# Optimization experiments

Hardware: AMD Instinct MI355X
Metric: run time of the kernel (lower is better)

The kernel has to match this reference:

```python
import jax, jax.numpy as jnp
import numpy as np

B, L, D = 4, 2048, 512
H, DK = 8, 64          # n_heads, d_k = d_model // n_heads
DF = 2048              # d_ff
W = 9                  # window_size (odd so padding w//2 keeps L windows)


def setup_inputs() -> dict:
    key = jax.random.key(0)
    ks = jax.random.split(key, 12)
    s = 0.02
    p = lambda k, shp: (jax.random.normal(k, shp, jnp.float32) * s)
    return {
        "x": jax.random.normal(ks[0], (B, L, D), jnp.float32),
        "Wq": p(ks[1], (D, D)), "bq": jnp.zeros((D,), jnp.float32),
        "Wk": p(ks[2], (D, D)), "bk": jnp.zeros((D,), jnp.float32),
        "Wv": p(ks[3], (D, D)), "bv": jnp.zeros((D,), jnp.float32),
        "Wo": p(ks[4], (D, D)), "bo": jnp.zeros((D,), jnp.float32),
        "W1": p(ks[5], (D, DF)), "b1": jnp.zeros((DF,), jnp.float32),
        "W2": p(ks[6], (DF, D)), "b2": jnp.zeros((D,), jnp.float32),
        "g1": jnp.ones((D,), jnp.float32), "be1": jnp.zeros((D,), jnp.float32),
        "g2": jnp.ones((D,), jnp.float32), "be2": jnp.zeros((D,), jnp.float32),
    }


def _layer_norm(x, g, b, eps=1e-5):
    m = jnp.mean(x, axis=-1, keepdims=True)
    v = jnp.var(x, axis=-1, keepdims=True)
    return (x - m) * jax.lax.rsqrt(v + eps) * g + b


def reference(x, Wq, bq, Wk, bk, Wv, bv, Wo, bo, W1, b1, W2, b2, g1, be1, g2, be2):
    b, l, d = x.shape
    pad = W // 2
    padded = jnp.pad(x, ((0, 0), (pad, pad), (0, 0)))          # (B, L+W-1, D)
    idx = jnp.arange(l)[:, None] + jnp.arange(W)[None, :]       # (L, W)
    win = padded[:, idx]                                        # (B, L, W, D)

    # per-window full attention (Informer FullAttention, mask_flag=False)
    q = (win @ Wq + bq).reshape(b, l, W, H, DK)
    k = (win @ Wk + bk).reshape(b, l, W, H, DK)
    v = (win @ Wv + bv).reshape(b, l, W, H, DK)
    scale = 1.0 / jnp.sqrt(jnp.float32(DK))
    scores = jnp.einsum('blqhe,blkhe->blhqk', q, k) * scale     # (B, L, H, W, W)
    attn = jax.nn.softmax(scores, axis=-1)
    o = jnp.einsum('blhqk,blkhd->blqhd', attn, v).reshape(b, l, W, d)
    o = o @ Wo + bo                                             # (B, L, W, D)
    new_x = jnp.mean(o, axis=2)                                 # mean-pool over window

    x1 = _layer_norm(x + new_x, g1, be1)

    # pointwise conv FFN (kernel_size=1 Conv1d == Linear), exact GELU
    h = jax.nn.gelu(x1 @ W1 + b1, approximate=False)
    y = h @ W2 + b2
    return _layer_norm(x1 + y, g2, be2)
```

## Files before the change

### kernel.cpp

```cpp
#include <hip/hip_runtime.h>


typedef unsigned short u16;
typedef __attribute__((ext_vector_type(8))) short short8;
typedef __attribute__((ext_vector_type(4))) float floatx4;

#define DEV static __device__ __forceinline__

DEV float b2f(u16 u) {
  union { unsigned int i; float f; } x; x.i = ((unsigned int)u) << 16; return x.f;
}
DEV u16 f2b(float f) {
  union { float f; unsigned int i; } x; x.f = f;
  unsigned int u = x.i + 0x7fffu + ((x.i >> 16) & 1u);
  return (u16)(u >> 16);
}

#define AS1 __attribute__((address_space(1)))
#define AS3 __attribute__((address_space(3)))
DEV void gload_lds16(const void* g, void* l) {
  __builtin_amdgcn_global_load_lds((const AS1 void*)g, (AS3 void*)l, 16, 0, 0);
}

__global__ __launch_bounds__(256) void prep_all(
    const float* __restrict__ Wq, const float* __restrict__ Wk,
    const float* __restrict__ Wo, const float* __restrict__ W1,
    const float* __restrict__ W2, const float* __restrict__ Wv,
    const float* __restrict__ bq, const float* __restrict__ bk,
    const float* __restrict__ bv, const float* __restrict__ x,
    u16* __restrict__ WqkvT, u16* __restrict__ WoT,
    u16* __restrict__ W1T, u16* __restrict__ W2T, u16* __restrict__ Wvb,
    float* __restrict__ bqkv, u16* __restrict__ xb) {
  const int bid = blockIdx.x;
  if (bid >= 3080) {
    const int i = (bid - 3080) * 256 + threadIdx.x;
    float4 v = ((const float4*)x)[i];
    ushort4 o;
    o.x = f2b(v.x); o.y = f2b(v.y); o.z = f2b(v.z); o.w = f2b(v.w);
    ((ushort4*)xb)[i] = o;
    return;
  }
  if (bid >= 3072) {
    const int i = (bid - 3072) * 256 + threadIdx.x;
    if (i < 512) bqkv[i] = bq[i];
    else if (i < 1024) bqkv[i] = bk[i - 512];
    else if (i < 1536) {
      const int c = i - 1024;
      float s = 0.f;
      for (int j = 0; j < 512; ++j) s += bv[j] * Wo[(size_t)j * 512 + c];
      bqkv[i] = s;
    } else bqkv[i] = 0.f;
    return;
  }
  if (bid >= 2816) {
    const int i = (bid - 2816) * 256 + threadIdx.x;
    float4 v = ((const float4*)Wv)[i];
    ushort4 o;
    o.x = f2b(v.x); o.y = f2b(v.y); o.z = f2b(v.z); o.w = f2b(v.w);
    ((ushort4*)Wvb)[i] = o;
    return;
  }
  const float* in; u16* out; int R, C, t;
  if (bid < 256)       { in = Wq; out = WqkvT;          R = 512;  C = 512;  t = bid; }
  else if (bid < 512)  { in = Wk; out = WqkvT + 262144; R = 512;  C = 512;  t = bid - 256; }
  else if (bid < 768)  { in = Wo; out = WoT;            R = 512;  C = 512;  t = bid - 512; }
  else if (bid < 1792) { in = W1; out = W1T;            R = 512;  C = 2048; t = bid - 768; }
  else                 { in = W2; out = W2T;            R = 2048; C = 512;  t = bid - 1792; }
  const int tpr = C >> 5;
  const int bc = (t % tpr) * 32, br = (t / tpr) * 32;
  __shared__ float tile[32][33];
  const int tx = threadIdx.x & 31, ty = threadIdx.x >> 5;
  #pragma unroll
  for (int i = 0; i < 32; i += 8)
    tile[ty + i][tx] = in[(size_t)(br + ty + i) * C + bc + tx];
  __syncthreads();
  #pragma unroll
  for (int i = 0; i < 32; i += 8)
    out[(size_t)(bc + ty + i) * R + br + tx] = f2b(tile[tx][ty + i]);
}

template<int EPI>
__global__ __launch_bounds__(256, 3) void gemm_bt(
    const u16* __restrict__ A, const u16* __restrict__ BT,
    const float* __restrict__ bias, u16* __restrict__ C,
    int M, int N, int lda, int kb) {
  __shared__ __align__(16) u16 As[2][8192];
  __shared__ __align__(16) u16 Bs[2][4096];
  const int tid = threadIdx.x;
  const int w = tid >> 6, l = tid & 63;
  const int l15 = l & 15, l4 = l >> 4;
  const int wr = w & 1, wc = w >> 1;

  const int gx = (int)gridDim.x, gy = (int)gridDim.y;
  int id = (int)blockIdx.y * gx + (int)blockIdx.x;
  const int nwg = gx * gy;
  if ((nwg & 7) == 0) { const int cpx = nwg >> 3; id = (id & 7) * cpx + (id >> 3); }
  const int bx = id % gx; const int by = id / gx;
  const int bm = by * 128, bn = bx * 64;

  const int srow = tid >> 3;
  const int sg8 = (((tid & 7) - (srow & 7)) & 7) * 8;
  const u16* gA = A  + (size_t)(bm + srow) * lda + sg8;
  const u16* gB = BT + (size_t)(bn + srow) * lda + sg8;
  const size_t r32 = (size_t)32 * lda;
  const int sd = tid * 8;

  int aOff[2][4], bOff[2][2];
  #pragma unroll
  for (int kh = 0; kh < 2; ++kh) {
    #pragma unroll
    for (int m = 0; m < 4; ++m) {
      const int r = wr * 64 + m * 16 + l15;
      aOff[kh][m] = r * 64 + (((l4 + 4 * kh) + (r & 7)) & 7) * 8;
    }
    #pragma unroll
    for (int n = 0; n < 2; ++n) {
      const int r = wc * 32 + n * 16 + l15;
      bOff[kh][n] = r * 64 + (((l4 + 4 * kh) + (r & 7)) & 7) * 8;
    }
  }

  floatx4 acc[4][2] = {};
  const int nt = kb >> 6;

  auto stage = [&](int t, int buf) {
    const u16* a = gA + (size_t)t * 64;
    const u16* b = gB + (size_t)t * 64;
    gload_lds16(a,           &As[buf][sd]);
    gload_lds16(a + r32,     &As[buf][2048 + sd]);
    gload_lds16(a + 2 * r32, &As[buf][4096 + sd]);
    gload_lds16(a + 3 * r32, &As[buf][6144 + sd]);
    gload_lds16(b,           &Bs[buf][sd]);
    gload_lds16(b + r32,     &Bs[buf][2048 + sd]);
  };

  stage(0, 0);
  asm volatile("s_waitcnt vmcnt(0)" ::: "memory");
  __builtin_amdgcn_s_barrier();
  asm volatile("" ::: "memory");

  for (int t = 0; t < nt; ++t) {
    const int cur = t & 1;
    if (t + 1 < nt) stage(t + 1, cur ^ 1);

    #pragma unroll
    for (int kh = 0; kh < 2; ++kh) {
      short8 af[4], bf[2];
      #pragma unroll
      for (int m = 0; m < 4; ++m) af[m] = *(const short8*)(&As[cur][aOff[kh][m]]);
      #pragma unroll
      for (int n = 0; n < 2; ++n) bf[n] = *(const short8*)(&Bs[cur][bOff[kh][n]]);
      #pragma unroll
      for (int m = 0; m < 4; ++m)
        #pragma unroll
        for (int n = 0; n < 2; ++n)
          acc[m][n] = __builtin_amdgcn_mfma_f32_16x16x32_bf16(af[m], bf[n], acc[m][n], 0, 0, 0);
    }

    asm volatile("s_waitcnt vmcnt(0)" ::: "memory");
    __builtin_amdgcn_s_barrier();
    asm volatile("" ::: "memory");
  }

  const int col0 = bn + wc * 32 + l15;
  float bvv[2];
  #pragma unroll
  for (int n = 0; n < 2; ++n) bvv[n] = bias[col0 + n * 16];
  #pragma unroll
  for (int m = 0; m < 4; ++m) {
    #pragma unroll
    for (int ri = 0; ri < 4; ++ri) {
      const size_t row = (size_t)(bm + wr * 64 + m * 16 + l4 * 4 + ri);
      u16* cp = C + row * N + col0;
      #pragma unroll
      for (int n = 0; n < 2; ++n) {
        float vv = acc[m][n][ri] + bvv[n];
        if (EPI == 1) {
          const float u = vv * (1.0f + 0.044715f * vv * vv);
          vv = vv / (1.0f + __expf(-1.5957691216057308f * u));
        }
        cp[n * 16] = f2b(vv);
      }
    }
  }
}

#define ATL 32
#define ART (ATL + 8)

__global__ __launch_bounds__(256) void attn_band(
    const u16* __restrict__ QKV, const float* __restrict__ bqkv,
    const float* __restrict__ bo, u16* __restrict__ newx) {
  __shared__ __align__(16) u16 S3[3][ART][72];
  __shared__ float Gb[ART][18];
  __shared__ float Sm[ART][81];
  __shared__ float Wb[ATL][9];

  const int tid = threadIdx.x;
  const int bid = ((int)blockIdx.x & 7) * 256 + ((int)blockIdx.x >> 3);
  const int h = bid & 7;
  const int chunk = (bid >> 3) & 63;
  const int b = bid >> 9;
  const int l0 = chunk * ATL;

  for (int idx = tid; idx < ART * 24; idx += 256) {
    const int ti = idx / 24, c = idx % 24;
    const int slice = c >> 3, d8 = (c & 7) * 8;
    const int col = slice * 512 + h * 64 + d8;
    const int t = l0 - 4 + ti;
    short8 v;
    if ((unsigned)t < 2048u) {
      v = *(const short8*)(QKV + ((size_t)((b << 11) | t)) * 1536 + col);
    } else {
      #pragma unroll
      for (int j = 0; j < 8; ++j) v[j] = (short)f2b(bqkv[col + j]);
    }
    *(short8*)(&S3[slice][ti][d8]) = v;
  }
  __syncthreads();

  for (int task = tid; task < ART * 17; task += 256) {
    const int ti = task / 17, j = task % 17;
    const int ui = ti + j - 8;
    if ((unsigned)ui < (unsigned)ART) {
      float a = 0.f;
      #pragma unroll
      for (int d0 = 0; d0 < 64; d0 += 8) {
        short8 qv = *(const short8*)(&S3[0][ti][d0]);
        short8 kv = *(const short8*)(&S3[1][ui][d0]);
        #pragma unroll
        for (int jj = 0; jj < 8; ++jj) a += b2f((u16)qv[jj]) * b2f((u16)kv[jj]);
      }
      Gb[ti][j] = a * 0.125f;
    }
  }
  __syncthreads();

  for (int task = tid; task < ART * 9; task += 256) {
    const int ti = task / 9, qw = task % 9;
    const int li = ti - qw;
    if ((unsigned)li < (unsigned)ATL) {
      float m = -1e30f;
      #pragma unroll
      for (int kw = 0; kw < 9; ++kw) m = fmaxf(m, Gb[ti][kw - qw + 8]);
      float e[9], s = 0.f;
      #pragma unroll
      for (int kw = 0; kw < 9; ++kw) { e[kw] = expf(Gb[ti][kw - qw + 8] - m); s += e[kw]; }
      const float inv = 1.f / s;
      #pragma unroll
      for (int kw = 0; kw < 9; ++kw) Sm[ti][qw * 9 + kw] = e[kw] * inv;
    }
  }
  __syncthreads();

  for (int task = tid; task < ATL * 9; task += 256) {
    const int li = task / 9, kw = task % 9;
    float s = 0.f;
    #pragma unroll
    for (int qw = 0; qw < 9; ++qw) s += Sm[li + qw][qw * 9 + kw];
    Wb[li][kw] = s * (1.f / 9.f);
  }
  __syncthreads();

  {
    const int li = tid >> 3, d8 = (tid & 7) * 8;
    float w[9];
    #pragma unroll
    for (int kw = 0; kw < 9; ++kw) w[kw] = Wb[li][kw];
    float a[8] = {};
    #pragma unroll
    for (int kw = 0; kw < 9; ++kw) {
      short8 vv = *(const short8*)(&S3[2][li + kw][d8]);
      #pragma unroll
      for (int jj = 0; jj < 8; ++jj) a[jj] += w[kw] * b2f((u16)vv[jj]);
    }
    short8 o;
    #pragma unroll
    for (int jj = 0; jj < 8; ++jj) o[jj] = (short)f2b(a[jj] + bo[h * 64 + d8 + jj]);
    const int l = l0 + li;
    *(short8*)(newx + ((size_t)((b << 11) | l)) * 512 + h * 64 + d8) = o;
  }
}

template<int MODE>
__global__ __launch_bounds__(256) void ln_kernel(
    const u16* __restrict__ a, const u16* __restrict__ bsrc,
    const float* __restrict__ g, const float* __restrict__ be,
    u16* __restrict__ outb, float* __restrict__ outf) {
  const int wave = threadIdx.x >> 6, lane = threadIdx.x & 63;
  const size_t row = (size_t)blockIdx.x * 4 + wave;
  const size_t base = row * 512 + lane * 8;
  const int gi = lane * 8;
  float v[8];
  short8 a8 = *(const short8*)(a + base);
  short8 b8 = *(const short8*)(bsrc + base);
  #pragma unroll
  for (int j = 0; j < 8; ++j) v[j] = b2f((u16)a8[j]) + b2f((u16)b8[j]);

  float s = 0.f;
  #pragma unroll
  for (int j = 0; j < 8; ++j) s += v[j];
  #pragma unroll
  for (int off = 32; off >= 1; off >>= 1) s += __shfl_xor(s, off, 64);
  const float mean = s * (1.f / 512.f);
  float sq = 0.f;
  #pragma unroll
  for (int j = 0; j < 8; ++j) { float d = v[j] - mean; sq += d * d; }
  #pragma unroll
  for (int off = 32; off >= 1; off >>= 1) sq += __shfl_xor(sq, off, 64);
  const float rs = rsqrtf(sq * (1.f / 512.f) + 1e-5f);

  if (MODE == 0) {
    short8 o;
    #pragma unroll
    for (int j = 0; j < 8; ++j)
      o[j] = (short)f2b((v[j] - mean) * rs * g[gi + j] + be[gi + j]);
    *(short8*)(outb + base) = o;
  } else {
    float4 o0, o1;
    o0.x = (v[0] - mean) * rs * g[gi + 0] + be[gi + 0];
    o0.y = (v[1] - mean) * rs * g[gi + 1] + be[gi + 1];
    o0.z = (v[2] - mean) * rs * g[gi + 2] + be[gi + 2];
    o0.w = (v[3] - mean) * rs * g[gi + 3] + be[gi + 3];
    o1.x = (v[4] - mean) * rs * g[gi + 4] + be[gi + 4];
    o1.y = (v[5] - mean) * rs * g[gi + 5] + be[gi + 5];
    o1.z = (v[6] - mean) * rs * g[gi + 6] + be[gi + 6];
    o1.w = (v[7] - mean) * rs * g[gi + 7] + be[gi + 7];
    *(float4*)(outf + base) = o0;
    *(float4*)(outf + base + 4) = o1;
  }
}

extern "C" void kernel_launch(void* const* d_in, const int* in_sizes, int n_in,
                              void* d_out, int out_size, void* d_ws, size_t ws_size,
                              hipStream_t stream) {
  const float* x   = (const float*)d_in[0];
  const float* Wq  = (const float*)d_in[1];
  const float* bq  = (const float*)d_in[2];
  const float* Wk  = (const float*)d_in[3];
  const float* bk  = (const float*)d_in[4];
  const float* Wv  = (const float*)d_in[5];
  const float* bv  = (const float*)d_in[6];
  const float* Wo  = (const float*)d_in[7];
  const float* bo  = (const float*)d_in[8];
  const float* W1  = (const float*)d_in[9];
  const float* b1  = (const float*)d_in[10];
  const float* W2  = (const float*)d_in[11];
  const float* b2  = (const float*)d_in[12];
  const float* g1  = (const float*)d_in[13];
  const float* be1 = (const float*)d_in[14];
  const float* g2  = (const float*)d_in[15];
  const float* be2 = (const float*)d_in[16];

  char* w = (char*)d_ws;
  u16*   xb    = (u16*)  (w + 0);
  u16*   WqkvT = (u16*)  (w + 8388608);
  u16*   WoT   = (u16*)  (w + 9961472);
  u16*   W1T   = (u16*)  (w + 10485760);
  u16*   W2T   = (u16*)  (w + 12582912);
  float* bqkv  = (float*)(w + 14680064);
  u16*   Wvb   = (u16*)  (w + 14688256);
  u16*   QKV   = (u16*)  (w + 15212544);
  u16*   hbuf  = QKV;
  u16*   newx  = (u16*)  (w + 48766976);
  u16*   x1b   = (u16*)  (w + 57155584);
  u16*   WvoT  = WqkvT + 524288;
  u16*   ybuf  = newx;

  prep_all<<<7176, 256, 0, stream>>>(Wq, Wk, Wo, W1, W2, Wv, bq, bk, bv, x,
                                     WqkvT, WoT, W1T, W2T, Wvb, bqkv, xb);
  gemm_bt<0><<<dim3(8, 4), 256, 0, stream>>>(WoT, Wvb, bqkv + 1536, WvoT,
                                             512, 512, 512, 512);
  gemm_bt<0><<<dim3(24, 64), 256, 0, stream>>>(xb, WqkvT, bqkv, QKV,
                                               8192, 1536, 512, 512);
  attn_band<<<2048, 256, 0, stream>>>(QKV, bqkv, bo, newx);
  ln_kernel<0><<<2048, 256, 0, stream>>>(xb, newx, g1, be1, x1b, nullptr);
  gemm_bt<1><<<dim3(32, 64), 256, 0, stream>>>(x1b, W1T, b1, hbuf,
                                               8192, 2048, 512, 512);
  gemm_bt<0><<<dim3(8, 64), 256, 0, stream>>>(hbuf, W2T, b2, ybuf,
                                              8192, 512, 2048, 2048);
  ln_kernel<1><<<2048, 256, 0, stream>>>(x1b, ybuf, g2, be2, nullptr, (float*)d_out);
}
```

Measured before the change: 145.0 us.

## Enlarge GEMM tiles to 256x128 and split-K the FFN down-projection

Replaces the 128x64 GEMM tile (BK=64) with a 256x128 tile (BK=32), where each wave holds an 8x4 MFMA accumulator block, so more MFMA work is done per LDS load. The second FFN GEMM (K=2048) is split into two K halves across gridDim.z, which writes two bf16 partial outputs. The final layernorm kernel sums those partials and adds the bias. This is meant to raise arithmetic intensity and keep enough blocks for the small-N GEMM, at the cost of more registers, lower occupancy, fewer blocks on the other GEMMs, and extra partial-sum traffic with bf16 rounding of each partial.

```diff
diff --git a/kernel.cpp b/kernel.cpp
--- a/kernel.cpp
+++ b/kernel.cpp
@@ -80,9 +80,9 @@
 }
 
 template<int EPI>
-__global__ __launch_bounds__(256, 3) void gemm_bt(
+__global__ __launch_bounds__(256, 2) void gemm_big(
     const u16* __restrict__ A, const u16* __restrict__ BT,
-    const float* __restrict__ bias, u16* __restrict__ C,
+    const float* __restrict__ bias, u16* __restrict__ C, u16* __restrict__ C2,
     int M, int N, int lda, int kb) {
   __shared__ __align__(16) u16 As[2][8192];
   __shared__ __align__(16) u16 Bs[2][4096];
@@ -92,46 +92,40 @@
   const int wr = w & 1, wc = w >> 1;
 
   const int gx = (int)gridDim.x, gy = (int)gridDim.y;
-  int id = (int)blockIdx.y * gx + (int)blockIdx.x;
-  const int nwg = gx * gy;
+  int id = ((int)blockIdx.z * gy + (int)blockIdx.y) * gx + (int)blockIdx.x;
+  const int nwg = gx * gy * (int)gridDim.z;
   if ((nwg & 7) == 0) { const int cpx = nwg >> 3; id = (id & 7) * cpx + (id >> 3); }
-  const int bx = id % gx; const int by = id / gx;
-  const int bm = by * 128, bn = bx * 64;
-
-  const int srow = tid >> 3;
-  const int sg8 = (((tid & 7) - (srow & 7)) & 7) * 8;
-  const u16* gA = A  + (size_t)(bm + srow) * lda + sg8;
-  const u16* gB = BT + (size_t)(bn + srow) * lda + sg8;
-  const size_t r32 = (size_t)32 * lda;
+  const int bx = id % gx; const int r1 = id / gx;
+  const int by = r1 % gy; const int bz = r1 / gy;
+  const int bm = by * 256, bn = bx * 128;
+  const int koff = bz * kb;
+
+  const int row0 = tid >> 2;
+  const int kc0 = ((((tid & 3) - ((tid >> 3) & 3)) & 3)) * 8;
+  const u16* gA = A  + (size_t)(bm + row0) * lda + koff + kc0;
+  const u16* gB = BT + (size_t)(bn + row0) * lda + koff + kc0;
+  const size_t r64 = (size_t)64 * lda;
   const int sd = tid * 8;
 
-  int aOff[2][4], bOff[2][2];
-  #pragma unroll
-  for (int kh = 0; kh < 2; ++kh) {
-    #pragma unroll
-    for (int m = 0; m < 4; ++m) {
-      const int r = wr * 64 + m * 16 + l15;
-      aOff[kh][m] = r * 64 + (((l4 + 4 * kh) + (r & 7)) & 7) * 8;
-    }
-    #pragma unroll
-    for (int n = 0; n < 2; ++n) {
-      const int r = wc * 32 + n * 16 + l15;
-      bOff[kh][n] = r * 64 + (((l4 + 4 * kh) + (r & 7)) & 7) * 8;
-    }
-  }
-
-  floatx4 acc[4][2] = {};
-  const int nt = kb >> 6;
+  const int rg8 = ((l4 + ((l15 >> 1) & 3)) & 3) * 8;
+  int aOff[8], bOff[4];
+  #pragma unroll
+  for (int m = 0; m < 8; ++m) aOff[m] = (wr * 128 + m * 16 + l15) * 32 + rg8;
+  #pragma unroll
+  for (int n = 0; n < 4; ++n) bOff[n] = (wc * 64 + n * 16 + l15) * 32 + rg8;
+
+  floatx4 acc[8][4] = {};
+  const int nt = kb >> 5;
 
   auto stage = [&](int t, int buf) {
-    const u16* a = gA + (size_t)t * 64;
-    const u16* b = gB + (size_t)t * 64;
+    const u16* a = gA + (size_t)t * 32;
+    const u16* b = gB + (size_t)t * 32;
     gload_lds16(a,           &As[buf][sd]);
-    gload_lds16(a + r32,     &As[buf][2048 + sd]);
-    gload_lds16(a + 2 * r32, &As[buf][4096 + sd]);
-    gload_lds16(a + 3 * r32, &As[buf][6144 + sd]);
+    gload_lds16(a + r64,     &As[buf][2048 + sd]);
+    gload_lds16(a + 2 * r64, &As[buf][4096 + sd]);
+    gload_lds16(a + 3 * r64, &As[buf][6144 + sd]);
     gload_lds16(b,           &Bs[buf][sd]);
-    gload_lds16(b + r32,     &Bs[buf][2048 + sd]);
+    gload_lds16(b + r64,     &Bs[buf][2048 + sd]);
   };
 
   stage(0, 0);
@@ -143,43 +137,54 @@
     const int cur = t & 1;
     if (t + 1 < nt) stage(t + 1, cur ^ 1);
 
-    #pragma unroll
-    for (int kh = 0; kh < 2; ++kh) {
-      short8 af[4], bf[2];
-      #pragma unroll
-      for (int m = 0; m < 4; ++m) af[m] = *(const short8*)(&As[cur][aOff[kh][m]]);
-      #pragma unroll
-      for (int n = 0; n < 2; ++n) bf[n] = *(const short8*)(&Bs[cur][bOff[kh][n]]);
-      #pragma unroll
-      for (int m = 0; m < 4; ++m)
-        #pragma unroll
-        for (int n = 0; n < 2; ++n)
-          acc[m][n] = __builtin_amdgcn_mfma_f32_16x16x32_bf16(af[m], bf[n], acc[m][n], 0, 0, 0);
-    }
+    short8 af[8], bf[4];
+    #pragma unroll
+    for (int m = 0; m < 8; ++m) af[m] = *(const short8*)(&As[cur][aOff[m]]);
+    #pragma unroll
+    for (int n = 0; n < 4; ++n) bf[n] = *(const short8*)(&Bs[cur][bOff[n]]);
+    #pragma unroll
+    for (int m = 0; m < 8; ++m)
+      #pragma unroll
+      for (int n = 0; n < 4; ++n)
+        acc[m][n] = __builtin_amdgcn_mfma_f32_16x16x32_bf16(af[m], bf[n], acc[m][n], 0, 0, 0);
 
     asm volatile("s_waitcnt vmcnt(0)" ::: "memory");
     __builtin_amdgcn_s_barrier();
     asm volatile("" ::: "memory");
   }
 
-  const int col0 = bn + wc * 32 + l15;
-  float bvv[2];
-  #pragma unroll
-  for (int n = 0; n < 2; ++n) bvv[n] = bias[col0 + n * 16];
-  #pragma unroll
-  for (int m = 0; m < 4; ++m) {
-    #pragma unroll
-    for (int ri = 0; ri < 4; ++ri) {
-      const size_t row = (size_t)(bm + wr * 64 + m * 16 + l4 * 4 + ri);
-      u16* cp = C + row * N + col0;
-      #pragma unroll
-      for (int n = 0; n < 2; ++n) {
-        float vv = acc[m][n][ri] + bvv[n];
-        if (EPI == 1) {
-          const float u = vv * (1.0f + 0.044715f * vv * vv);
-          vv = vv / (1.0f + __expf(-1.5957691216057308f * u));
+  const int col0 = bn + wc * 64 + l15;
+  if (EPI <= 1) {
+    float bvv[4];
+    #pragma unroll
+    for (int n = 0; n < 4; ++n) bvv[n] = bias[col0 + n * 16];
+    #pragma unroll
+    for (int m = 0; m < 8; ++m) {
+      #pragma unroll
+      for (int ri = 0; ri < 4; ++ri) {
+        const size_t row = (size_t)(bm + wr * 128 + m * 16 + l4 * 4 + ri);
+        u16* cp = C + row * N + col0;
+        #pragma unroll
+        for (int n = 0; n < 4; ++n) {
+          float vv = acc[m][n][ri] + bvv[n];
+          if (EPI == 1) {
+            const float u = vv * (1.0f + 0.044715f * vv * vv);
+            vv = vv / (1.0f + __expf(-1.5957691216057308f * u));
+          }
+          cp[n * 16] = f2b(vv);
         }
-        cp[n * 16] = f2b(vv);
+      }
+    }
+  } else {
+    u16* o = (bz == 0) ? C : C2;
+    #pragma unroll
+    for (int m = 0; m < 8; ++m) {
+      #pragma unroll
+      for (int ri = 0; ri < 4; ++ri) {
+        const size_t row = (size_t)(bm + wr * 128 + m * 16 + l4 * 4 + ri);
+        u16* cp = o + row * N + col0;
+        #pragma unroll
+        for (int n = 0; n < 4; ++n) cp[n * 16] = f2b(acc[m][n][ri]);
       }
     }
   }
@@ -285,6 +290,7 @@
 template<int MODE>
 __global__ __launch_bounds__(256) void ln_kernel(
     const u16* __restrict__ a, const u16* __restrict__ bsrc,
+    const u16* __restrict__ csrc, const float* __restrict__ bias,
     const float* __restrict__ g, const float* __restrict__ be,
     u16* __restrict__ outb, float* __restrict__ outf) {
   const int wave = threadIdx.x >> 6, lane = threadIdx.x & 63;
@@ -296,6 +302,11 @@
   short8 b8 = *(const short8*)(bsrc + base);
   #pragma unroll
   for (int j = 0; j < 8; ++j) v[j] = b2f((u16)a8[j]) + b2f((u16)b8[j]);
+  if (MODE == 1) {
+    short8 c8 = *(const short8*)(csrc + base);
+    #pragma unroll
+    for (int j = 0; j < 8; ++j) v[j] += b2f((u16)c8[j]) + bias[gi + j];
+  }
 
   float s = 0.f;
   #pragma unroll
@@ -365,19 +376,20 @@
   u16*   newx  = (u16*)  (w + 48766976);
   u16*   x1b   = (u16*)  (w + 57155584);
   u16*   WvoT  = WqkvT + 524288;
-  u16*   ybuf  = newx;
+  u16*   yp0   = newx;
+  u16*   yp1   = xb;
 
   prep_all<<<7176, 256, 0, stream>>>(Wq, Wk, Wo, W1, W2, Wv, bq, bk, bv, x,
                                      WqkvT, WoT, W1T, W2T, Wvb, bqkv, xb);
-  gemm_bt<0><<<dim3(8, 4), 256, 0, stream>>>(WoT, Wvb, bqkv + 1536, WvoT,
-                                             512, 512, 512, 512);
-  gemm_bt<0><<<dim3(24, 64), 256, 0, stream>>>(xb, WqkvT, bqkv, QKV,
-                                               8192, 1536, 512, 512);
+  gemm_big<0><<<dim3(4, 2, 1), 256, 0, stream>>>(WoT, Wvb, bqkv + 1536, WvoT, nullptr,
+                                                 512, 512, 512, 512);
+  gemm_big<0><<<dim3(12, 32, 1), 256, 0, stream>>>(xb, WqkvT, bqkv, QKV, nullptr,
+                                                   8192, 1536, 512, 512);
   attn_band<<<2048, 256, 0, stream>>>(QKV, bqkv, bo, newx);
-  ln_kernel<0><<<2048, 256, 0, stream>>>(xb, newx, g1, be1, x1b, nullptr);
-  gemm_bt<1><<<dim3(32, 64), 256, 0, stream>>>(x1b, W1T, b1, hbuf,
-                                               8192, 2048, 512, 512);
-  gemm_bt<0><<<dim3(8, 64), 256, 0, stream>>>(hbuf, W2T, b2, ybuf,
-                                              8192, 512, 2048, 2048);
-  ln_kernel<1><<<2048, 256, 0, stream>>>(x1b, ybuf, g2, be2, nullptr, (float*)d_out);
-}
+  ln_kernel<0><<<2048, 256, 0, stream>>>(xb, newx, nullptr, nullptr, g1, be1, x1b, nullptr);
+  gemm_big<1><<<dim3(16, 32, 1), 256, 0, stream>>>(x1b, W1T, b1, hbuf, nullptr,
+                                                   8192, 2048, 512, 512);
+  gemm_big<2><<<dim3(4, 32, 2), 256, 0, stream>>>(hbuf, W2T, nullptr, yp0, yp1,
+                                                  8192, 512, 2048, 1024);
+  ln_kernel<1><<<2048, 256, 0, stream>>>(x1b, yp0, yp1, b2, g2, be2, nullptr, (float*)d_out);
+}
```

After: 164.9 us. 13.7% more time.

## Split-K the W2 GEMM and load B fragments directly into registers

Applied to the files above, without the earlier changes.

The GEMM kernel no longer stages B tiles in LDS. Each wave loads its B fragments straight from global memory into registers, prefetched one K-step ahead. A grid z-dimension adds split-K: the W2 GEMM now runs as two K halves that write bf16 partials to two buffers, and the second LayerNorm sums both partials and adds the bias. This doubles the block count of the narrow W2 GEMM to improve occupancy and halves LDS use per block. The cost is extra partial-buffer traffic, an extra bf16 rounding of partial sums, and uncoalesced global B loads.

```diff
diff --git a/kernel.cpp b/kernel.cpp
--- a/kernel.cpp
+++ b/kernel.cpp
@@ -82,104 +82,135 @@
 template<int EPI>
 __global__ __launch_bounds__(256, 3) void gemm_bt(
     const u16* __restrict__ A, const u16* __restrict__ BT,
-    const float* __restrict__ bias, u16* __restrict__ C,
+    const float* __restrict__ bias, u16* __restrict__ C, u16* __restrict__ C2,
     int M, int N, int lda, int kb) {
   __shared__ __align__(16) u16 As[2][8192];
-  __shared__ __align__(16) u16 Bs[2][4096];
   const int tid = threadIdx.x;
   const int w = tid >> 6, l = tid & 63;
   const int l15 = l & 15, l4 = l >> 4;
   const int wr = w & 1, wc = w >> 1;
 
   const int gx = (int)gridDim.x, gy = (int)gridDim.y;
-  int id = (int)blockIdx.y * gx + (int)blockIdx.x;
-  const int nwg = gx * gy;
+  int id = ((int)blockIdx.z * gy + (int)blockIdx.y) * gx + (int)blockIdx.x;
+  const int nwg = gx * gy * (int)gridDim.z;
   if ((nwg & 7) == 0) { const int cpx = nwg >> 3; id = (id & 7) * cpx + (id >> 3); }
-  const int bx = id % gx; const int by = id / gx;
+  const int bx = id % gx; const int r1 = id / gx;
+  const int by = r1 % gy; const int bz = r1 / gy;
   const int bm = by * 128, bn = bx * 64;
+  const int koff = bz * kb;
 
   const int srow = tid >> 3;
   const int sg8 = (((tid & 7) - (srow & 7)) & 7) * 8;
-  const u16* gA = A  + (size_t)(bm + srow) * lda + sg8;
-  const u16* gB = BT + (size_t)(bn + srow) * lda + sg8;
+  const u16* gA = A + (size_t)(bm + srow) * lda + koff + sg8;
   const size_t r32 = (size_t)32 * lda;
   const int sd = tid * 8;
 
-  int aOff[2][4], bOff[2][2];
-  #pragma unroll
-  for (int kh = 0; kh < 2; ++kh) {
+  int aOff[2][4];
+  #pragma unroll
+  for (int kh = 0; kh < 2; ++kh)
     #pragma unroll
     for (int m = 0; m < 4; ++m) {
       const int r = wr * 64 + m * 16 + l15;
       aOff[kh][m] = r * 64 + (((l4 + 4 * kh) + (r & 7)) & 7) * 8;
     }
-    #pragma unroll
-    for (int n = 0; n < 2; ++n) {
-      const int r = wc * 32 + n * 16 + l15;
-      bOff[kh][n] = r * 64 + (((l4 + 4 * kh) + (r & 7)) & 7) * 8;
-    }
-  }
+
+  const u16* pB = BT + (size_t)(bn + wc * 32 + l15) * lda + koff + l4 * 8;
+  const size_t bn16 = (size_t)16 * lda;
 
   floatx4 acc[4][2] = {};
   const int nt = kb >> 6;
 
-  auto stage = [&](int t, int buf) {
+  auto stageA = [&](int t, int buf) {
     const u16* a = gA + (size_t)t * 64;
-    const u16* b = gB + (size_t)t * 64;
     gload_lds16(a,           &As[buf][sd]);
     gload_lds16(a + r32,     &As[buf][2048 + sd]);
     gload_lds16(a + 2 * r32, &As[buf][4096 + sd]);
     gload_lds16(a + 3 * r32, &As[buf][6144 + sd]);
-    gload_lds16(b,           &Bs[buf][sd]);
-    gload_lds16(b + r32,     &Bs[buf][2048 + sd]);
   };
 
-  stage(0, 0);
+  short8 b00, b01, b10, b11, n00, n01, n10, n11;
+  b00 = *(const short8*)(pB);
+  b01 = *(const short8*)(pB + bn16);
+  b10 = *(const short8*)(pB + 32);
+  b11 = *(const short8*)(pB + bn16 + 32);
+
+  stageA(0, 0);
   asm volatile("s_waitcnt vmcnt(0)" ::: "memory");
   __builtin_amdgcn_s_barrier();
   asm volatile("" ::: "memory");
 
   for (int t = 0; t < nt; ++t) {
     const int cur = t & 1;
-    if (t + 1 < nt) stage(t + 1, cur ^ 1);
-
-    #pragma unroll
-    for (int kh = 0; kh < 2; ++kh) {
-      short8 af[4], bf[2];
-      #pragma unroll
-      for (int m = 0; m < 4; ++m) af[m] = *(const short8*)(&As[cur][aOff[kh][m]]);
-      #pragma unroll
-      for (int n = 0; n < 2; ++n) bf[n] = *(const short8*)(&Bs[cur][bOff[kh][n]]);
-      #pragma unroll
-      for (int m = 0; m < 4; ++m)
-        #pragma unroll
-        for (int n = 0; n < 2; ++n)
-          acc[m][n] = __builtin_amdgcn_mfma_f32_16x16x32_bf16(af[m], bf[n], acc[m][n], 0, 0, 0);
+    const bool pf = (t + 1 < nt);
+    if (pf) {
+      stageA(t + 1, cur ^ 1);
+      const u16* pb = pB + (size_t)(t + 1) * 64;
+      n00 = *(const short8*)(pb);
+      n01 = *(const short8*)(pb + bn16);
+      n10 = *(const short8*)(pb + 32);
+      n11 = *(const short8*)(pb + bn16 + 32);
+    }
+
+    {
+      short8 af[4];
+      #pragma unroll
+      for (int m = 0; m < 4; ++m) af[m] = *(const short8*)(&As[cur][aOff[0][m]]);
+      #pragma unroll
+      for (int m = 0; m < 4; ++m) {
+        acc[m][0] = __builtin_amdgcn_mfma_f32_16x16x32_bf16(af[m], b00, acc[m][0], 0, 0, 0);
+        acc[m][1] = __builtin_amdgcn_mfma_f32_16x16x32_bf16(af[m], b01, acc[m][1], 0, 0, 0);
+      }
+    }
+    {
+      short8 af[4];
+      #pragma unroll
+      for (int m = 0; m < 4; ++m) af[m] = *(const short8*)(&As[cur][aOff[1][m]]);
+      #pragma unroll
+      for (int m = 0; m < 4; ++m) {
+        acc[m][0] = __builtin_amdgcn_mfma_f32_16x16x32_bf16(af[m], b10, acc[m][0], 0, 0, 0);
+        acc[m][1] = __builtin_amdgcn_mfma_f32_16x16x32_bf16(af[m], b11, acc[m][1], 0, 0, 0);
+      }
     }
 
     asm volatile("s_waitcnt vmcnt(0)" ::: "memory");
     __builtin_amdgcn_s_barrier();
     asm volatile("" ::: "memory");
+
+    if (pf) { b00 = n00; b01 = n01; b10 = n10; b11 = n11; }
   }
 
   const int col0 = bn + wc * 32 + l15;
-  float bvv[2];
-  #pragma unroll
-  for (int n = 0; n < 2; ++n) bvv[n] = bias[col0 + n * 16];
-  #pragma unroll
-  for (int m = 0; m < 4; ++m) {
-    #pragma unroll
-    for (int ri = 0; ri < 4; ++ri) {
-      const size_t row = (size_t)(bm + wr * 64 + m * 16 + l4 * 4 + ri);
-      u16* cp = C + row * N + col0;
-      #pragma unroll
-      for (int n = 0; n < 2; ++n) {
-        float vv = acc[m][n][ri] + bvv[n];
-        if (EPI == 1) {
-          const float u = vv * (1.0f + 0.044715f * vv * vv);
-          vv = vv / (1.0f + __expf(-1.5957691216057308f * u));
+  if (EPI <= 1) {
+    float bvv[2];
+    #pragma unroll
+    for (int n = 0; n < 2; ++n) bvv[n] = bias[col0 + n * 16];
+    #pragma unroll
+    for (int m = 0; m < 4; ++m) {
+      #pragma unroll
+      for (int ri = 0; ri < 4; ++ri) {
+        const size_t row = (size_t)(bm + wr * 64 + m * 16 + l4 * 4 + ri);
+        u16* cp = C + row * N + col0;
+        #pragma unroll
+        for (int n = 0; n < 2; ++n) {
+          float vv = acc[m][n][ri] + bvv[n];
+          if (EPI == 1) {
+            const float u = vv * (1.0f + 0.044715f * vv * vv);
+            vv = vv / (1.0f + __expf(-1.5957691216057308f * u));
+          }
+          cp[n * 16] = f2b(vv);
         }
-        cp[n * 16] = f2b(vv);
+      }
+    }
+  } else {
+    u16* o = (bz == 0) ? C : C2;
+    #pragma unroll
+    for (int m = 0; m < 4; ++m) {
+      #pragma unroll
+      for (int ri = 0; ri < 4; ++ri) {
+        const size_t row = (size_t)(bm + wr * 64 + m * 16 + l4 * 4 + ri);
+        u16* cp = o + row * N + col0;
+        #pragma unroll
+        for (int n = 0; n < 2; ++n) cp[n * 16] = f2b(acc[m][n][ri]);
       }
     }
   }
@@ -285,6 +316,7 @@
 template<int MODE>
 __global__ __launch_bounds__(256) void ln_kernel(
     const u16* __restrict__ a, const u16* __restrict__ bsrc,
+    const u16* __restrict__ csrc, const float* __restrict__ bias,
     const float* __restrict__ g, const float* __restrict__ be,
     u16* __restrict__ outb, float* __restrict__ outf) {
   const int wave = threadIdx.x >> 6, lane = threadIdx.x & 63;
@@ -296,6 +328,11 @@
   short8 b8 = *(const short8*)(bsrc + base);
   #pragma unroll
   for (int j = 0; j < 8; ++j) v[j] = b2f((u16)a8[j]) + b2f((u16)b8[j]);
+  if (MODE == 1) {
+    short8 c8 = *(const short8*)(csrc + base);
+    #pragma unroll
+    for (int j = 0; j < 8; ++j) v[j] += b2f((u16)c8[j]) + bias[gi + j];
+  }
 
   float s = 0.f;
   #pragma unroll
@@ -365,19 +402,20 @@
   u16*   newx  = (u16*)  (w + 48766976);
   u16*   x1b   = (u16*)  (w + 57155584);
   u16*   WvoT  = WqkvT + 524288;
-  u16*   ybuf  = newx;
+  u16*   yp0   = newx;
+  u16*   yp1   = xb;
 
   prep_all<<<7176, 256, 0, stream>>>(Wq, Wk, Wo, W1, W2, Wv, bq, bk, bv, x,
                                      WqkvT, WoT, W1T, W2T, Wvb, bqkv, xb);
-  gemm_bt<0><<<dim3(8, 4), 256, 0, stream>>>(WoT, Wvb, bqkv + 1536, WvoT,
-                                             512, 512, 512, 512);
-  gemm_bt<0><<<dim3(24, 64), 256, 0, stream>>>(xb, WqkvT, bqkv, QKV,
-                                               8192, 1536, 512, 512);
+  gemm_bt<0><<<dim3(8, 4, 1), 256, 0, stream>>>(WoT, Wvb, bqkv + 1536, WvoT, nullptr,
+                                                512, 512, 512, 512);
+  gemm_bt<0><<<dim3(24, 64, 1), 256, 0, stream>>>(xb, WqkvT, bqkv, QKV, nullptr,
+                                                  8192, 1536, 512, 512);
   attn_band<<<2048, 256, 0, stream>>>(QKV, bqkv, bo, newx);
-  ln_kernel<0><<<2048, 256, 0, stream>>>(xb, newx, g1, be1, x1b, nullptr);
-  gemm_bt<1><<<dim3(32, 64), 256, 0, stream>>>(x1b, W1T, b1, hbuf,
-                                               8192, 2048, 512, 512);
-  gemm_bt<0><<<dim3(8, 64), 256, 0, stream>>>(hbuf, W2T, b2, ybuf,
-                                              8192, 512, 2048, 2048);
-  ln_kernel<1><<<2048, 256, 0, stream>>>(x1b, ybuf, g2, be2, nullptr, (float*)d_out);
-}
+  ln_kernel<0><<<2048, 256, 0, stream>>>(xb, newx, nullptr, nullptr, g1, be1, x1b, nullptr);
+  gemm_bt<1><<<dim3(32, 64, 1), 256, 0, stream>>>(x1b, W1T, b1, hbuf, nullptr,
+                                                  8192, 2048, 512, 512);
+  gemm_bt<2><<<dim3(8, 64, 2), 256, 0, stream>>>(hbuf, W2T, nullptr, yp0, yp1,
+                                                 8192, 512, 2048, 1024);
+  ln_kernel<1><<<2048, 256, 0, stream>>>(x1b, yp0, yp1, b2, g2, be2, nullptr, (float*)d_out);
+}
```

Measured after the change: 191.1 us. +31.8%, slower.
